# Kernel optimization log

Hardware: AMD Instinct MI355X
Metric: run time of the kernel (lower is better)

Reference implementation:

```python
import jax, jax.numpy as jnp
import numpy as np

LN_EPS = 1e-5  # torch LayerNorm default


def setup_inputs() -> dict:
    key = jax.random.key(0)
    k1, k2, k3 = jax.random.split(key, 3)
    B, L, D = 8, 2048, 1024
    CS, CD = 8192, 16
    x = jax.random.normal(k1, (B, L, D), dtype=jnp.float32)
    # xavier_uniform for Linear(dim, codebook_dim): bound = sqrt(6/(fan_in+fan_out))
    bound = float(np.sqrt(6.0 / (D + CD)))
    W = jax.random.uniform(k2, (CD, D), dtype=jnp.float32, minval=-bound, maxval=bound)
    codebook = jax.random.normal(k3, (CS, CD), dtype=jnp.float32)
    return {"x": x, "W": W, "codebook": codebook}


def reference(x, W, codebook):
    # random projection: (B,L,D) @ (D,CD) -> (B,L,CD)
    z = jnp.einsum("bld,cd->blc", x, W)
    # LayerNorm over last dim, no affine
    mu = jnp.mean(z, axis=-1, keepdims=True)
    var = jnp.mean(jnp.square(z - mu), axis=-1, keepdims=True)
    z = (z - mu) / jnp.sqrt(var + LN_EPS)
    # squared euclidean distance via matmul decomposition (avoids (B,L,CS,CD) tensor):
    # ||z - c||^2 = ||z||^2 - 2 z.c + ||c||^2 ; argmin is identical to argmin of the norm
    z_sq = jnp.sum(jnp.square(z), axis=-1, keepdims=True)        # (B,L,1)
    c_sq = jnp.sum(jnp.square(codebook), axis=-1)                # (CS,)
    d2 = z_sq - 2.0 * jnp.einsum("blc,kc->blk", z, codebook) + c_sq  # (B,L,CS)
    codes = jnp.argmin(d2, axis=-1)                              # (B,L) int32
    return codes
```

## Files before the change

### kernel.cpp

```cpp
#include <hip/hip_runtime.h>
#include <math.h>

#define D      1024
#define CD     16
#define CS     8192
#define ROWS   16384
#define LN_EPS 1e-5f
#define KCHUNK 512
#define NCHUNK (CS / KCHUNK)
#define KSPLIT 4

typedef __attribute__((ext_vector_type(8))) short short8;
typedef __attribute__((ext_vector_type(4))) float f32x4;

__device__ inline unsigned short bf16_rne(float v) {
    unsigned u = __float_as_uint(v);
    unsigned r = u + 0x7FFFu + ((u >> 16) & 1u);
    return (unsigned short)(r >> 16);
}
__device__ inline float bf16_f(unsigned short s) {
    return __uint_as_float(((unsigned)s) << 16);
}
__device__ inline short8 ld8(const unsigned short* p) { return *(const short8*)p; }

__device__ inline void split3(float v, unsigned short& a, unsigned short& b, unsigned short& c) {
    unsigned u = __float_as_uint(v);
    unsigned r = u + 0x7FFFu + ((u >> 16) & 1u);
    a = (unsigned short)(r >> 16);
    float r1 = v - __uint_as_float(r & 0xFFFF0000u);
    unsigned u1 = __float_as_uint(r1);
    unsigned r1b = u1 + 0x7FFFu + ((u1 >> 16) & 1u);
    b = (unsigned short)(r1b >> 16);
    float r2 = r1 - __uint_as_float(r1b & 0xFFFF0000u);
    c = bf16_rne(r2);
}

__global__ __launch_bounds__(256) void pack_w(const float* __restrict__ W,
                                              unsigned short* __restrict__ wb)
{
    int tid = blockIdx.x * 256 + threadIdx.x;
    int gk   = tid / 192;
    int rem  = tid % 192;
    int term = rem >> 6;
    int L    = rem & 63;
    int n = L & 15, q = L >> 4;
    const float* src = W + n * D + gk * 32 + q * 8;
    unsigned short* dst = wb + (size_t)tid * 8;
    #pragma unroll
    for (int j = 0; j < 8; ++j) {
        unsigned short h0, h1, h2;
        split3(src[j], h0, h1, h2);
        dst[j] = term == 0 ? h0 : (term == 1 ? h1 : h2);
    }
}

__global__ __launch_bounds__(256) void projA(const float* __restrict__ x,
                                             const unsigned short* __restrict__ wb,
                                             float* __restrict__ zpart)
{
    const int t = threadIdx.x;
    const int L = t & 63;
    const int kq = t >> 6;
    const int rt = blockIdx.x;
    const int m = L & 15, q = L >> 4;
    const float* xrow = x + (size_t)(rt * 16 + m) * D + kq * 256 + q * 8;
    const unsigned short* wbase = wb + (size_t)(kq * 8) * 1536;

    f32x4 acc = {0.f, 0.f, 0.f, 0.f};
    #pragma unroll 2
    for (int kk = 0; kk < 8; ++kk) {
        float4 xa = *(const float4*)(xrow + kk * 32);
        float4 xb = *(const float4*)(xrow + kk * 32 + 4);
        const unsigned short* wp = wbase + (size_t)kk * 1536 + L * 8;
        short8 w0 = ld8(wp);
        short8 w1 = ld8(wp + 512);
        short8 w2 = ld8(wp + 1024);
        float vs[8] = {xa.x, xa.y, xa.z, xa.w, xb.x, xb.y, xb.z, xb.w};
        short8 x0, x1, x2;
        #pragma unroll
        for (int j = 0; j < 8; ++j) {
            unsigned short h0, h1, h2;
            split3(vs[j], h0, h1, h2);
            x0[j] = (short)h0; x1[j] = (short)h1; x2[j] = (short)h2;
        }
        acc = __builtin_amdgcn_mfma_f32_16x16x32_bf16(x0, w0, acc, 0, 0, 0);
        acc = __builtin_amdgcn_mfma_f32_16x16x32_bf16(x0, w1, acc, 0, 0, 0);
        acc = __builtin_amdgcn_mfma_f32_16x16x32_bf16(x1, w0, acc, 0, 0, 0);
        acc = __builtin_amdgcn_mfma_f32_16x16x32_bf16(x1, w1, acc, 0, 0, 0);
        acc = __builtin_amdgcn_mfma_f32_16x16x32_bf16(x0, w2, acc, 0, 0, 0);
        acc = __builtin_amdgcn_mfma_f32_16x16x32_bf16(x2, w0, acc, 0, 0, 0);
    }
    #pragma unroll
    for (int r = 0; r < 4; ++r)
        zpart[((size_t)kq * ROWS + rt * 16 + q * 4 + r) * CD + m] = acc[r];
}

__global__ __launch_bounds__(256) void projB(const float* __restrict__ zpart,
                                             unsigned short* __restrict__ zp)
{
    const int t = threadIdx.x;
    const int c = t & 15;
    const int rl = t >> 4;
    const size_t row = (size_t)blockIdx.x * 16 + rl;
    float z = 0.f;
    #pragma unroll
    for (int kq = 0; kq < KSPLIT; ++kq)
        z += zpart[((size_t)kq * ROWS + row) * CD + c];

    float s = z;
    for (int m = 1; m < 16; m <<= 1) s += __shfl_xor(s, m, 64);
    float mu = s * (1.f / 16.f);
    float d  = z - mu;
    float v2 = d * d;
    for (int m = 1; m < 16; m <<= 1) v2 += __shfl_xor(v2, m, 64);
    float var = v2 * (1.f / 16.f);
    float zn = d / sqrtf(var + LN_EPS);

    unsigned short h0, h1, h2;
    split3(zn, h0, h1, h2);
    unsigned short* zr = zp + row * 48;
    zr[c] = h0; zr[16 + c] = h1; zr[32 + c] = h2;
}

__global__ __launch_bounds__(256) void pack_cb(const float* __restrict__ cb,
                                               unsigned short* __restrict__ cbp,
                                               float* __restrict__ nhc)
{
    int k = blockIdx.x * 256 + threadIdx.x;
    const float* c = cb + (long)k * CD;
    unsigned short* o = cbp + (long)k * 48;
    float csq = 0.f;
    #pragma unroll
    for (int d = 0; d < 16; ++d) {
        float v = c[d];
        csq = fmaf(v, v, csq);
        unsigned short h0, h1, h2;
        split3(v, h0, h1, h2);
        o[d] = h0; o[16 + d] = h1; o[32 + d] = h2;
    }
    nhc[k] = -0.5f * csq;
}

__global__ __launch_bounds__(512, 4) void dist_argmin(const unsigned short* __restrict__ zp,
                                                      const unsigned short* __restrict__ cbp,
                                                      const float* __restrict__ nhc,
                                                      float* __restrict__ pbest,
                                                      int* __restrict__ pidx)
{
    __shared__ __align__(16) unsigned short cl[KCHUNK * 48];
    __shared__ float ql[KCHUNK];
    const int t = threadIdx.x;
    const int kbase = blockIdx.y * KCHUNK;

    {
        float4* dst = (float4*)cl;
        const float4* src = (const float4*)(cbp + (size_t)kbase * 48);
        #pragma unroll
        for (int i = 0; i < 6; ++i) dst[t + i * 512] = src[t + i * 512];
        if (t < KCHUNK / 4) ((float4*)ql)[t] = ((const float4*)(nhc + kbase))[t];
    }
    __syncthreads();

    const int L = t & 63;
    const int w = t >> 6;
    const int n = L & 15;
    const int q = L >> 4;

    short8 a1[4], a2[4];
    const int rt0 = blockIdx.x * 32 + w * 4;
    #pragma unroll
    for (int j = 0; j < 4; ++j) {
        const unsigned short* zr = zp + (size_t)((rt0 + j) * 16 + n) * 48;
        a1[j] = ld8(zr + q * 8);
        a2[j] = ld8(zr + (q < 2 ? q * 8 : 16 + q * 8));
    }

    float best[4][4];
    int   bi[4][4];
    #pragma unroll
    for (int j = 0; j < 4; ++j)
        #pragma unroll
        for (int r = 0; r < 4; ++r) { best[j][r] = -INFINITY; bi[j][r] = 0; }

    const int o1 = q * 8;
    const int o2 = (q * 8 + 16) & 31;
    const int o3 = q < 2 ? 32 + q * 8 : (q - 2) * 8;

    for (int tt = 0; tt < KCHUNK / 16; ++tt) {
        const unsigned short* cb_t = cl + (size_t)(tt * 16 + n) * 48;
        short8 b1 = ld8(cb_t + o1);
        short8 b2 = ld8(cb_t + o2);
        short8 b3 = ld8(cb_t + o3);
        float bneg = ql[tt * 16 + n];
        int code = kbase + tt * 16 + n;
        f32x4 acc[4];
        #pragma unroll
        for (int j = 0; j < 4; ++j) acc[j] = (f32x4){bneg, bneg, bneg, bneg};
        #pragma unroll
        for (int j = 0; j < 4; ++j)
            acc[j] = __builtin_amdgcn_mfma_f32_16x16x32_bf16(a1[j], b1, acc[j], 0, 0, 0);
        #pragma unroll
        for (int j = 0; j < 4; ++j)
            acc[j] = __builtin_amdgcn_mfma_f32_16x16x32_bf16(a1[j], b2, acc[j], 0, 0, 0);
        #pragma unroll
        for (int j = 0; j < 4; ++j)
            acc[j] = __builtin_amdgcn_mfma_f32_16x16x32_bf16(a2[j], b3, acc[j], 0, 0, 0);
        #pragma unroll
        for (int j = 0; j < 4; ++j)
            #pragma unroll
            for (int r = 0; r < 4; ++r)
                if (acc[j][r] > best[j][r]) { best[j][r] = acc[j][r]; bi[j][r] = code; }
    }

    #pragma unroll
    for (int mask = 1; mask < 16; mask <<= 1) {
        #pragma unroll
        for (int j = 0; j < 4; ++j)
            #pragma unroll
            for (int r = 0; r < 4; ++r) {
                float s2 = __shfl_xor(best[j][r], mask, 64);
                int   i2 = __shfl_xor(bi[j][r], mask, 64);
                if (s2 > best[j][r] || (s2 == best[j][r] && i2 < bi[j][r])) {
                    best[j][r] = s2; bi[j][r] = i2;
                }
            }
    }
    if (n == 0) {
        #pragma unroll
        for (int j = 0; j < 4; ++j)
            #pragma unroll
            for (int r = 0; r < 4; ++r) {
                int row = (rt0 + j) * 16 + q * 4 + r;
                pbest[(size_t)row * NCHUNK + blockIdx.y] = best[j][r];
                pidx [(size_t)row * NCHUNK + blockIdx.y] = bi[j][r];
            }
    }
}

__global__ __launch_bounds__(256) void merge_argmin(const float* __restrict__ pbest,
                                                    const int* __restrict__ pidx,
                                                    int* __restrict__ out)
{
    const long row = (long)blockIdx.x * 256 + threadIdx.x;
    float best = -INFINITY;
    int   bi   = 0;
    #pragma unroll
    for (int i = 0; i < NCHUNK; ++i) {
        float s = pbest[row * NCHUNK + i];
        if (s > best) { best = s; bi = pidx[row * NCHUNK + i]; }
    }
    out[row] = bi;
}

extern "C" void kernel_launch(void* const* d_in, const int* in_sizes, int n_in,
                              void* d_out, int out_size, void* d_ws, size_t ws_size,
                              hipStream_t stream)
{
    const float* x  = (const float*)d_in[0];
    const float* W  = (const float*)d_in[1];
    const float* cb = (const float*)d_in[2];
    int* out = (int*)d_out;

    char* ws = (char*)d_ws;
    unsigned short* zp  = (unsigned short*)ws;
    unsigned short* cbp = (unsigned short*)(ws + 0x180000);
    float* nhc  = (float*)(ws + 0x240000);
    unsigned short* wb = (unsigned short*)(ws + 0x248000);
    float* zpart = (float*)(ws + 0x260000);
    float* pbest = (float*)(ws + 0x260000);
    int*   pidx  = (int*)  (ws + 0x360000);

    pack_w <<<24, 256, 0, stream>>>(W, wb);
    pack_cb<<<CS / 256, 256, 0, stream>>>(cb, cbp, nhc);
    projA  <<<ROWS / 16, 256, 0, stream>>>(x, wb, zpart);
    projB  <<<ROWS / 16, 256, 0, stream>>>(zpart, zp);
    dist_argmin<<<dim3(32, NCHUNK), 512, 0, stream>>>(zp, cbp, nhc, pbest, pidx);
    merge_argmin<<<ROWS / 256, 256, 0, stream>>>(pbest, pidx, out);
}
```

Measured before the change: 142.7 us.

## Fuse projection with LayerNorm, merge pack kernels, and cut codebook LDS loads

Combines pack_w and pack_cb into one launch. Fuses projA and projB into proj_ln, which splits K across two waves and reduces the halves through shared memory before doing LayerNorm in registers. This removes the zpart round trip through global memory and two kernel launches. In dist_argmin the z-side split terms are preloaded into a third register set, so each codebook tile needs two LDS vector loads instead of three, at the cost of more VGPRs.

```diff
diff --git a/kernel.cpp b/kernel.cpp
--- a/kernel.cpp
+++ b/kernel.cpp
@@ -8,7 +8,6 @@
 #define LN_EPS 1e-5f
 #define KCHUNK 512
 #define NCHUNK (CS / KCHUNK)
-#define KSPLIT 4
 
 typedef __attribute__((ext_vector_type(8))) short short8;
 typedef __attribute__((ext_vector_type(4))) float f32x4;
@@ -17,9 +16,6 @@
     unsigned u = __float_as_uint(v);
     unsigned r = u + 0x7FFFu + ((u >> 16) & 1u);
     return (unsigned short)(r >> 16);
-}
-__device__ inline float bf16_f(unsigned short s) {
-    return __uint_as_float(((unsigned)s) << 16);
 }
 __device__ inline short8 ld8(const unsigned short* p) { return *(const short8*)p; }
 
@@ -35,40 +31,64 @@
     c = bf16_rne(r2);
 }
 
-__global__ __launch_bounds__(256) void pack_w(const float* __restrict__ W,
-                                              unsigned short* __restrict__ wb)
-{
-    int tid = blockIdx.x * 256 + threadIdx.x;
-    int gk   = tid / 192;
-    int rem  = tid % 192;
-    int term = rem >> 6;
-    int L    = rem & 63;
-    int n = L & 15, q = L >> 4;
-    const float* src = W + n * D + gk * 32 + q * 8;
-    unsigned short* dst = wb + (size_t)tid * 8;
-    #pragma unroll
-    for (int j = 0; j < 8; ++j) {
-        unsigned short h0, h1, h2;
-        split3(src[j], h0, h1, h2);
-        dst[j] = term == 0 ? h0 : (term == 1 ? h1 : h2);
-    }
-}
-
-__global__ __launch_bounds__(256) void projA(const float* __restrict__ x,
-                                             const unsigned short* __restrict__ wb,
-                                             float* __restrict__ zpart)
-{
+__global__ __launch_bounds__(256) void pack_all(const float* __restrict__ W,
+                                                const float* __restrict__ cb,
+                                                unsigned short* __restrict__ wb,
+                                                unsigned short* __restrict__ cbp,
+                                                float* __restrict__ nhc)
+{
+    const int t = threadIdx.x;
+    if (blockIdx.x < 32) {
+        int k = blockIdx.x * 256 + t;
+        const float* c = cb + (long)k * CD;
+        unsigned short* o = cbp + (long)k * 48;
+        float csq = 0.f;
+        #pragma unroll
+        for (int d = 0; d < 16; ++d) {
+            float v = c[d];
+            csq = fmaf(v, v, csq);
+            unsigned short h0, h1, h2;
+            split3(v, h0, h1, h2);
+            o[d] = h0; o[16 + d] = h1; o[32 + d] = h2;
+        }
+        nhc[k] = -0.5f * csq;
+    } else {
+        int tid = (blockIdx.x - 32) * 256 + t;
+        int gk   = tid / 192;
+        int rem  = tid % 192;
+        int term = rem >> 6;
+        int L    = rem & 63;
+        int n = L & 15, q = L >> 4;
+        const float* src = W + n * D + gk * 32 + q * 8;
+        unsigned short* dst = wb + (size_t)tid * 8;
+        #pragma unroll
+        for (int j = 0; j < 8; ++j) {
+            unsigned short h0, h1, h2;
+            split3(src[j], h0, h1, h2);
+            dst[j] = term == 0 ? h0 : (term == 1 ? h1 : h2);
+        }
+    }
+}
+
+__global__ __launch_bounds__(256, 4) void proj_ln(const float* __restrict__ x,
+                                                  const unsigned short* __restrict__ wb,
+                                                  unsigned short* __restrict__ zp)
+{
+    __shared__ float part[2][64][4];
     const int t = threadIdx.x;
     const int L = t & 63;
-    const int kq = t >> 6;
-    const int rt = blockIdx.x;
-    const int m = L & 15, q = L >> 4;
-    const float* xrow = x + (size_t)(rt * 16 + m) * D + kq * 256 + q * 8;
-    const unsigned short* wbase = wb + (size_t)(kq * 8) * 1536;
+    const int w = t >> 6;
+    const int tb = w & 1;
+    const int kh = w >> 1;
+    const int rt = blockIdx.x * 2 + tb;
+    const int n = L & 15, q = L >> 4;
+
+    const float* xrow = x + (size_t)(rt * 16 + n) * D + kh * 512 + q * 8;
+    const unsigned short* wbase = wb + (size_t)(kh * 16) * 1536;
 
     f32x4 acc = {0.f, 0.f, 0.f, 0.f};
-    #pragma unroll 2
-    for (int kk = 0; kk < 8; ++kk) {
+    #pragma unroll 4
+    for (int kk = 0; kk < 16; ++kk) {
         float4 xa = *(const float4*)(xrow + kk * 32);
         float4 xb = *(const float4*)(xrow + kk * 32 + 4);
         const unsigned short* wp = wbase + (size_t)kk * 1536 + L * 8;
@@ -90,55 +110,30 @@
         acc = __builtin_amdgcn_mfma_f32_16x16x32_bf16(x0, w2, acc, 0, 0, 0);
         acc = __builtin_amdgcn_mfma_f32_16x16x32_bf16(x2, w0, acc, 0, 0, 0);
     }
-    #pragma unroll
-    for (int r = 0; r < 4; ++r)
-        zpart[((size_t)kq * ROWS + rt * 16 + q * 4 + r) * CD + m] = acc[r];
-}
-
-__global__ __launch_bounds__(256) void projB(const float* __restrict__ zpart,
-                                             unsigned short* __restrict__ zp)
-{
-    const int t = threadIdx.x;
-    const int c = t & 15;
-    const int rl = t >> 4;
-    const size_t row = (size_t)blockIdx.x * 16 + rl;
-    float z = 0.f;
-    #pragma unroll
-    for (int kq = 0; kq < KSPLIT; ++kq)
-        z += zpart[((size_t)kq * ROWS + row) * CD + c];
-
-    float s = z;
-    for (int m = 1; m < 16; m <<= 1) s += __shfl_xor(s, m, 64);
-    float mu = s * (1.f / 16.f);
-    float d  = z - mu;
-    float v2 = d * d;
-    for (int m = 1; m < 16; m <<= 1) v2 += __shfl_xor(v2, m, 64);
-    float var = v2 * (1.f / 16.f);
-    float zn = d / sqrtf(var + LN_EPS);
-
-    unsigned short h0, h1, h2;
-    split3(zn, h0, h1, h2);
-    unsigned short* zr = zp + row * 48;
-    zr[c] = h0; zr[16 + c] = h1; zr[32 + c] = h2;
-}
-
-__global__ __launch_bounds__(256) void pack_cb(const float* __restrict__ cb,
-                                               unsigned short* __restrict__ cbp,
-                                               float* __restrict__ nhc)
-{
-    int k = blockIdx.x * 256 + threadIdx.x;
-    const float* c = cb + (long)k * CD;
-    unsigned short* o = cbp + (long)k * 48;
-    float csq = 0.f;
-    #pragma unroll
-    for (int d = 0; d < 16; ++d) {
-        float v = c[d];
-        csq = fmaf(v, v, csq);
-        unsigned short h0, h1, h2;
-        split3(v, h0, h1, h2);
-        o[d] = h0; o[16 + d] = h1; o[32 + d] = h2;
-    }
-    nhc[k] = -0.5f * csq;
+
+    if (kh == 1) {
+        #pragma unroll
+        for (int r = 0; r < 4; ++r) part[tb][L][r] = acc[r];
+    }
+    __syncthreads();
+    if (kh == 0) {
+        #pragma unroll
+        for (int r = 0; r < 4; ++r) {
+            float zv = acc[r] + part[tb][L][r];
+            float s = zv;
+            for (int m = 1; m < 16; m <<= 1) s += __shfl_xor(s, m, 64);
+            float mu = s * (1.f / 16.f);
+            float dd = zv - mu;
+            float v2 = dd * dd;
+            for (int m = 1; m < 16; m <<= 1) v2 += __shfl_xor(v2, m, 64);
+            float var = v2 * (1.f / 16.f);
+            float zn = dd / sqrtf(var + LN_EPS);
+            unsigned short h0, h1, h2;
+            split3(zn, h0, h1, h2);
+            unsigned short* zr = zp + (size_t)(rt * 16 + q * 4 + r) * 48;
+            zr[n] = h0; zr[16 + n] = h1; zr[32 + n] = h2;
+        }
+    }
 }
 
 __global__ __launch_bounds__(512, 4) void dist_argmin(const unsigned short* __restrict__ zp,
@@ -166,13 +161,18 @@
     const int n = L & 15;
     const int q = L >> 4;
 
-    short8 a1[4], a2[4];
+    const int oa2 = (q * 8 + 16) & 31;
+    const int oa3 = q < 2 ? 32 + q * 8 : (q - 2) * 8;
+    const int ob3 = q < 2 ? q * 8 : 16 + q * 8;
+
+    short8 a1[4], a2[4], a3[4];
     const int rt0 = blockIdx.x * 32 + w * 4;
     #pragma unroll
     for (int j = 0; j < 4; ++j) {
         const unsigned short* zr = zp + (size_t)((rt0 + j) * 16 + n) * 48;
         a1[j] = ld8(zr + q * 8);
-        a2[j] = ld8(zr + (q < 2 ? q * 8 : 16 + q * 8));
+        a2[j] = ld8(zr + oa2);
+        a3[j] = ld8(zr + oa3);
     }
 
     float best[4][4];
@@ -182,29 +182,23 @@
         #pragma unroll
         for (int r = 0; r < 4; ++r) { best[j][r] = -INFINITY; bi[j][r] = 0; }
 
-    const int o1 = q * 8;
-    const int o2 = (q * 8 + 16) & 31;
-    const int o3 = q < 2 ? 32 + q * 8 : (q - 2) * 8;
-
     for (int tt = 0; tt < KCHUNK / 16; ++tt) {
         const unsigned short* cb_t = cl + (size_t)(tt * 16 + n) * 48;
-        short8 b1 = ld8(cb_t + o1);
-        short8 b2 = ld8(cb_t + o2);
-        short8 b3 = ld8(cb_t + o3);
+        short8 b1 = ld8(cb_t + q * 8);
+        short8 b3 = ld8(cb_t + ob3);
         float bneg = ql[tt * 16 + n];
+        f32x4 bias = {bneg, bneg, bneg, bneg};
         int code = kbase + tt * 16 + n;
         f32x4 acc[4];
         #pragma unroll
-        for (int j = 0; j < 4; ++j) acc[j] = (f32x4){bneg, bneg, bneg, bneg};
-        #pragma unroll
-        for (int j = 0; j < 4; ++j)
-            acc[j] = __builtin_amdgcn_mfma_f32_16x16x32_bf16(a1[j], b1, acc[j], 0, 0, 0);
-        #pragma unroll
-        for (int j = 0; j < 4; ++j)
-            acc[j] = __builtin_amdgcn_mfma_f32_16x16x32_bf16(a1[j], b2, acc[j], 0, 0, 0);
-        #pragma unroll
-        for (int j = 0; j < 4; ++j)
-            acc[j] = __builtin_amdgcn_mfma_f32_16x16x32_bf16(a2[j], b3, acc[j], 0, 0, 0);
+        for (int j = 0; j < 4; ++j)
+            acc[j] = __builtin_amdgcn_mfma_f32_16x16x32_bf16(a1[j], b1, bias, 0, 0, 0);
+        #pragma unroll
+        for (int j = 0; j < 4; ++j)
+            acc[j] = __builtin_amdgcn_mfma_f32_16x16x32_bf16(a2[j], b1, acc[j], 0, 0, 0);
+        #pragma unroll
+        for (int j = 0; j < 4; ++j)
+            acc[j] = __builtin_amdgcn_mfma_f32_16x16x32_bf16(a3[j], b3, acc[j], 0, 0, 0);
         #pragma unroll
         for (int j = 0; j < 4; ++j)
             #pragma unroll
@@ -266,14 +260,11 @@
     unsigned short* cbp = (unsigned short*)(ws + 0x180000);
     float* nhc  = (float*)(ws + 0x240000);
     unsigned short* wb = (unsigned short*)(ws + 0x248000);
-    float* zpart = (float*)(ws + 0x260000);
     float* pbest = (float*)(ws + 0x260000);
     int*   pidx  = (int*)  (ws + 0x360000);
 
-    pack_w <<<24, 256, 0, stream>>>(W, wb);
-    pack_cb<<<CS / 256, 256, 0, stream>>>(cb, cbp, nhc);
-    projA  <<<ROWS / 16, 256, 0, stream>>>(x, wb, zpart);
-    projB  <<<ROWS / 16, 256, 0, stream>>>(zpart, zp);
+    pack_all<<<56, 256, 0, stream>>>(W, cb, wb, cbp, nhc);
+    proj_ln <<<ROWS / 32, 256, 0, stream>>>(x, wb, zp);
     dist_argmin<<<dim3(32, NCHUNK), 512, 0, stream>>>(zp, cbp, nhc, pbest, pidx);
     merge_argmin<<<ROWS / 256, 256, 0, stream>>>(pbest, pidx, out);
 }
```

Result: no change. 140.4 us (-1.6%).
